# Optimization experiments

Hardware: AMD Instinct MI355X
Metric: run time of the kernel (lower is better)

Reference implementation:

```python
import jax, jax.numpy as jnp
import numpy as np

N = 50000   # nodes
E = 600000  # edges
D = 128     # embedding_size (= in_size)
OUT = 2     # out_channels
L = 12
# aggr schedule from the source: conv1..conv10, conv11, con12
AGGRS = ['sum', 'mean', 'max', 'sum', 'mean', 'max', 'sum', 'mean', 'max', 'sum', 'max', 'mean']


def setup_inputs() -> dict:
    key = jax.random.key(0)
    ks = jax.random.split(key, 8)
    s = 1.0 / np.sqrt(D)
    x = jax.random.normal(ks[0], (N, D), jnp.float32)
    edge_index = jax.random.randint(ks[1], (2, E), 0, N, jnp.int32)
    # stacked SAGEConv params: lin_l (neighbor path, with bias), lin_r (root path, no bias)
    Wl = jax.random.normal(ks[2], (L, D, D), jnp.float32) * s
    bl = jax.random.normal(ks[3], (L, D), jnp.float32) * s
    Wr = jax.random.normal(ks[4], (L, D, D), jnp.float32) * s
    W1 = jax.random.normal(ks[5], (D, D), jnp.float32) * s
    b1 = jnp.zeros((D,), jnp.float32)
    W2 = jax.random.normal(ks[6], (OUT, D), jnp.float32) * s
    b2 = jnp.zeros((OUT,), jnp.float32)
    return {"x": x, "edge_index": edge_index, "Wl": Wl, "bl": bl, "Wr": Wr,
            "W1": W1, "b1": b1, "W2": W2, "b2": b2}


def _aggregate(msgs, dst, aggr):
    # msgs: [E, D] gathered source features; scatter-reduce to [N, D]
    if aggr == 'sum':
        return jax.ops.segment_sum(msgs, dst, num_segments=N)
    if aggr == 'mean':
        s = jax.ops.segment_sum(msgs, dst, num_segments=N)
        cnt = jax.ops.segment_sum(jnp.ones((msgs.shape[0], 1), msgs.dtype), dst, num_segments=N)
        return s / jnp.maximum(cnt, 1.0)
    # max: empty segments come back -inf -> 0 (PyG convention)
    mx = jax.ops.segment_max(msgs, dst, num_segments=N)
    return jnp.where(jnp.isneginf(mx), 0.0, mx)


def reference(x, edge_index, Wl, bl, Wr, W1, b1, W2, b2):
    src, dst = edge_index[0], edge_index[1]
    h = x
    for i, aggr in enumerate(AGGRS):
        agg = _aggregate(h[src], dst, aggr)          # gather + scatter-reduce
        h = jax.nn.relu(agg @ Wl[i].T + bl[i] + h @ Wr[i].T)
        # dropout after layers 10 and 11 is identity in eval mode
    h = jax.nn.relu(h @ W1.T + b1)
    return h @ W2.T + b2
```

## Files before the change

kernel.cpp:

```cpp
#include <hip/hip_runtime.h>
#include <math.h>

#define NN 50000
#define NE 600000
#define DIM 128
#define NL 12

typedef short bf16x8 __attribute__((ext_vector_type(8)));
typedef float f32x4 __attribute__((ext_vector_type(4)));

__device__ __forceinline__ uint f2b_rne(float f) {
    uint u = __float_as_uint(f);
    return (u + 0x7fffu + ((u >> 16) & 1u)) >> 16;
}

#define NX8 (NN * DIM / 8)
#define NW8 (NL * DIM * DIM / 8)
#define NW18 (DIM * DIM / 8)
#define NCVT (NX8 + 2 * NW8 + NW18)

__global__ void prep_kernel(const float* __restrict__ x, const float* __restrict__ Wl,
                            const float* __restrict__ Wr, const float* __restrict__ W1,
                            ushort* __restrict__ xb, ushort* __restrict__ Wlb,
                            ushort* __restrict__ Wrb, ushort* __restrict__ W1b,
                            const int* __restrict__ dst, int* __restrict__ counts) {
    int i = blockIdx.x * blockDim.x + threadIdx.x;
    if (i < NE) atomicAdd(&counts[dst[i]], 1);
    const float* in; ushort* out; int off;
    if (i < NX8)                        { in = x;  out = xb;  off = i; }
    else if (i < NX8 + NW8)             { in = Wl; out = Wlb; off = i - NX8; }
    else if (i < NX8 + 2 * NW8)         { in = Wr; out = Wrb; off = i - NX8 - NW8; }
    else if (i < NCVT)                  { in = W1; out = W1b; off = i - NX8 - 2 * NW8; }
    else return;
    const float4* p = reinterpret_cast<const float4*>(in);
    float4 v0 = p[off * 2], v1 = p[off * 2 + 1];
    uint4 o;
    o.x = (f2b_rne(v0.y) << 16) | f2b_rne(v0.x);
    o.y = (f2b_rne(v0.w) << 16) | f2b_rne(v0.z);
    o.z = (f2b_rne(v1.y) << 16) | f2b_rne(v1.x);
    o.w = (f2b_rne(v1.w) << 16) | f2b_rne(v1.z);
    reinterpret_cast<uint4*>(out)[off] = o;
}

__global__ __launch_bounds__(1024) void scan1_kernel(const int* __restrict__ counts,
                                                     int* __restrict__ offsets,
                                                     int* __restrict__ bsums) {
    int b = blockIdx.x, t = threadIdx.x;
    int i = b * 1024 + t;
    int lane = t & 63, wid = t >> 6;
    int val = (i < NN) ? counts[i] : 0;
#pragma unroll
    for (int o = 1; o < 64; o <<= 1) {
        int n = __shfl_up(val, o);
        if (lane >= o) val += n;
    }
    __shared__ int ws[16];
    if (lane == 63) ws[wid] = val;
    __syncthreads();
    if (wid == 0 && lane < 16) {
        int s = ws[lane];
#pragma unroll
        for (int o = 1; o < 16; o <<= 1) {
            int n = __shfl_up(s, o);
            if (lane >= o) s += n;
        }
        ws[lane] = s;
    }
    __syncthreads();
    if (wid) val += ws[wid - 1];
    if (i < NN) offsets[i + 1] = val;
    if (t == 1023) bsums[b] = val;
}

__global__ void scan2_kernel(const int* __restrict__ bsums, int* __restrict__ bbase, int nb) {
    int lane = threadIdx.x;
    int v = (lane < nb) ? bsums[lane] : 0;
    int val = v;
#pragma unroll
    for (int o = 1; o < 64; o <<= 1) {
        int n = __shfl_up(val, o);
        if (lane >= o) val += n;
    }
    if (lane < nb) bbase[lane] = val - v;
}

__global__ void scan3_kernel(int* __restrict__ offsets, const int* __restrict__ bbase) {
    int i = blockIdx.x * blockDim.x + threadIdx.x;
    if (i == 0) { offsets[0] = 0; return; }
    if (i <= NN) offsets[i] += bbase[(i - 1) >> 10];
}

__global__ void fill_kernel(const int* __restrict__ src, const int* __restrict__ dst,
                            const int* __restrict__ offsets, int* __restrict__ cursor,
                            int* __restrict__ csr) {
    int e = blockIdx.x * blockDim.x + threadIdx.x;
    if (e < NE) {
        int d = dst[e];
        int p = atomicAdd(&cursor[d], 1);
        csr[offsets[d] + p] = src[e];
    }
}

template <int AGGR>
__global__ __launch_bounds__(256) void aggregate_kernel(
    const ushort* __restrict__ h, ushort* __restrict__ agg,
    const int* __restrict__ csr, const int* __restrict__ offsets) {
    int wid = (blockIdx.x * blockDim.x + threadIdx.x) >> 6;
    int l = threadIdx.x & 63;
    if (wid >= NN) return;
    int s0 = offsets[wid], s1 = offsets[wid + 1];
    const uint* hp = reinterpret_cast<const uint*>(h);
    float ax, ay;
    if (AGGR == 2) { ax = ay = -INFINITY; } else { ax = ay = 0.f; }
    for (int e = s0; e < s1; e += 16) {
        int rem = s1 - e;
        uint u[16];
#pragma unroll
        for (int q = 0; q < 16; ++q) {
            int ee = (q < rem) ? e + q : s1 - 1;
            uint off = (uint)csr[ee] * 64u + (uint)l;
            u[q] = hp[off];
        }
        __builtin_amdgcn_sched_barrier(0);
#pragma unroll
        for (int q = 0; q < 16; ++q) {
            if (q < rem) {
                float fx = __uint_as_float(u[q] << 16);
                float fy = __uint_as_float(u[q] & 0xffff0000u);
                if (AGGR == 2) { ax = fmaxf(ax, fx); ay = fmaxf(ay, fy); }
                else           { ax += fx;           ay += fy; }
            }
        }
    }
    int deg = s1 - s0;
    if (AGGR == 1) {
        float inv = 1.f / (float)(deg > 0 ? deg : 1);
        ax *= inv; ay *= inv;
    }
    if (AGGR == 2 && deg == 0) { ax = ay = 0.f; }
    uint o = (f2b_rne(ay) << 16) | f2b_rne(ax);
    reinterpret_cast<uint*>(agg)[(uint)wid * 64u + (uint)l] = o;
}

template <int NPASS>
__global__ __launch_bounds__(256) void gemm_kernel(
    const ushort* __restrict__ A1, const ushort* __restrict__ Wa,
    const ushort* __restrict__ A2, const ushort* __restrict__ Wb,
    const float* __restrict__ bias, ushort* __restrict__ C) {
    __shared__ ushort Wlds[NPASS][DIM * DIM];
    int t = threadIdx.x, w = t >> 6, l = t & 63;
    int lr = l & 15, lg = l >> 4;

#pragma unroll
    for (int pass = 0; pass < NPASS; ++pass) {
        const uint4* Wv = reinterpret_cast<const uint4*>(pass ? Wb : Wa);
        char* base = reinterpret_cast<char*>(Wlds[pass]);
#pragma unroll
        for (int i = 0; i < 8; ++i) {
            int chunk = t + i * 256;
            uint4 v = Wv[chunk];
            int byte = chunk << 4;
            int row = byte >> 8;
            *reinterpret_cast<uint4*>(base + (byte ^ ((row & 7) << 4))) = v;
        }
    }
    __syncthreads();

    int row0 = blockIdx.x * 128 + w * 32;
    f32x4 acc[2][8];
#pragma unroll
    for (int rf = 0; rf < 2; ++rf)
#pragma unroll
        for (int c = 0; c < 8; ++c) acc[rf][c] = (f32x4){0.f, 0.f, 0.f, 0.f};
    int grow0 = min(row0 + lr, NN - 1);
    int grow1 = min(row0 + 16 + lr, NN - 1);

#pragma unroll
    for (int pass = 0; pass < NPASS; ++pass) {
        const ushort* A = pass ? A2 : A1;
        const char* wbase = reinterpret_cast<const char*>(Wlds[pass]);
#pragma unroll
        for (int kk = 0; kk < 4; ++kk) {
            int ko = kk * 32 + lg * 8;
            bf16x8 nf0 = *reinterpret_cast<const bf16x8*>(A + (size_t)grow0 * DIM + ko);
            bf16x8 nf1 = *reinterpret_cast<const bf16x8*>(A + (size_t)grow1 * DIM + ko);
#pragma unroll
            for (int c = 0; c < 8; ++c) {
                int wbyte = (((c * 16 + lr) << 8) + (ko << 1)) ^ ((lr & 7) << 4);
                bf16x8 wf = *reinterpret_cast<const bf16x8*>(wbase + wbyte);
                acc[0][c] = __builtin_amdgcn_mfma_f32_16x16x32_bf16(wf, nf0, acc[0][c], 0, 0, 0);
                acc[1][c] = __builtin_amdgcn_mfma_f32_16x16x32_bf16(wf, nf1, acc[1][c], 0, 0, 0);
            }
        }
    }
#pragma unroll
    for (int rf = 0; rf < 2; ++rf) {
        int orow = row0 + rf * 16 + lr;
        if (orow < NN) {
#pragma unroll
            for (int c = 0; c < 8; ++c) {
                int col0 = c * 16 + lg * 4;
                float4 b4 = *reinterpret_cast<const float4*>(bias + col0);
                float v0 = fmaxf(acc[rf][c][0] + b4.x, 0.f);
                float v1 = fmaxf(acc[rf][c][1] + b4.y, 0.f);
                float v2 = fmaxf(acc[rf][c][2] + b4.z, 0.f);
                float v3 = fmaxf(acc[rf][c][3] + b4.w, 0.f);
                uint2 o;
                o.x = (f2b_rne(v1) << 16) | f2b_rne(v0);
                o.y = (f2b_rne(v3) << 16) | f2b_rne(v2);
                *reinterpret_cast<uint2*>(C + (size_t)orow * DIM + col0) = o;
            }
        }
    }
}

__global__ void out_kernel(const ushort* __restrict__ h2, const float* __restrict__ W2,
                           const float* __restrict__ b2, float* __restrict__ out) {
    int wid = (blockIdx.x * blockDim.x + threadIdx.x) >> 6;
    int lane = threadIdx.x & 63;
    if (wid >= NN) return;
    uint u = reinterpret_cast<const uint*>(h2)[(uint)wid * 64u + (uint)lane];
    float vx = __uint_as_float(u << 16), vy = __uint_as_float(u & 0xffff0000u);
    float2 w0 = *reinterpret_cast<const float2*>(W2 + lane * 2);
    float2 w1 = *reinterpret_cast<const float2*>(W2 + DIM + lane * 2);
    float s0 = vx * w0.x + vy * w0.y;
    float s1 = vx * w1.x + vy * w1.y;
    for (int off = 32; off; off >>= 1) {
        s0 += __shfl_down(s0, off);
        s1 += __shfl_down(s1, off);
    }
    if (lane == 0) {
        out[wid * 2 + 0] = s0 + b2[0];
        out[wid * 2 + 1] = s1 + b2[1];
    }
}

extern "C" void kernel_launch(void* const* d_in, const int* in_sizes, int n_in,
                              void* d_out, int out_size, void* d_ws, size_t ws_size,
                              hipStream_t stream) {
    const float* x  = (const float*)d_in[0];
    const int*   ei = (const int*)d_in[1];
    const float* Wl = (const float*)d_in[2];
    const float* bl = (const float*)d_in[3];
    const float* Wr = (const float*)d_in[4];
    const float* W1 = (const float*)d_in[5];
    const float* b1 = (const float*)d_in[6];
    const float* W2 = (const float*)d_in[7];
    const float* b2 = (const float*)d_in[8];
    float* out = (float*)d_out;

    int* counts  = (int*)d_ws;
    int* offsets = counts + NN;
    int* bsums   = offsets + NN + 1;
    int* bbase   = bsums + 64;
    int* csr     = bbase + 64;
    size_t fixed = ((size_t)(NN + NN + 1 + 128 + NE) * sizeof(int) + 255) & ~(size_t)255;
    ushort* xb   = (ushort*)((char*)d_ws + fixed);
    ushort* bufA = xb + (size_t)NN * DIM;
    ushort* bufB = bufA + (size_t)NN * DIM;
    ushort* Wlb  = bufB + (size_t)NN * DIM;
    ushort* Wrb  = Wlb + (size_t)NL * DIM * DIM;
    ushort* W1b  = Wrb + (size_t)NL * DIM * DIM;

    const int* src = ei;
    const int* dst = ei + NE;

    hipMemsetAsync(counts, 0, NN * sizeof(int), stream);
    prep_kernel<<<(NCVT + 255) / 256, 256, 0, stream>>>(x, Wl, Wr, W1, xb, Wlb, Wrb, W1b,
                                                        dst, counts);
    const int NB = (NN + 1023) / 1024;
    scan1_kernel<<<NB, 1024, 0, stream>>>(counts, offsets, bsums);
    scan2_kernel<<<1, 64, 0, stream>>>(bsums, bbase, NB);
    scan3_kernel<<<(NN + 1 + 255) / 256, 256, 0, stream>>>(offsets, bbase);
    hipMemsetAsync(counts, 0, NN * sizeof(int), stream);
    fill_kernel<<<(NE + 255) / 256, 256, 0, stream>>>(src, dst, offsets, counts, csr);

    static const int AGGRS[NL] = {0, 1, 2, 0, 1, 2, 0, 1, 2, 0, 2, 1};
    dim3 agrd((NN * 64 + 255) / 256);
    dim3 ggrd((NN + 127) / 128);
    ushort* B[3] = {xb, bufA, bufB};
    int hi = 0;
    for (int i = 0; i < NL; ++i) {
        int ai = (hi + 1) % 3, oi = (hi + 2) % 3;
        const ushort* h = B[hi];
        if (AGGRS[i] == 0)
            aggregate_kernel<0><<<agrd, 256, 0, stream>>>(h, B[ai], csr, offsets);
        else if (AGGRS[i] == 1)
            aggregate_kernel<1><<<agrd, 256, 0, stream>>>(h, B[ai], csr, offsets);
        else
            aggregate_kernel<2><<<agrd, 256, 0, stream>>>(h, B[ai], csr, offsets);
        gemm_kernel<2><<<ggrd, 256, 0, stream>>>(B[ai], Wlb + (size_t)i * DIM * DIM, h,
                                                 Wrb + (size_t)i * DIM * DIM,
                                                 bl + (size_t)i * DIM, B[oi]);
        hi = oi;
    }
    int fi = (hi + 1) % 3;
    gemm_kernel<1><<<ggrd, 256, 0, stream>>>(B[hi], W1b, nullptr, nullptr, b1, B[fi]);
    out_kernel<<<agrd, 256, 0, stream>>>(B[fi], W2, b2, out);
}
```

Baseline: 614.7 us.

## Process two nodes per wave in aggregation and reuse single LDS weight buffer in GEMM

The aggregation kernel now assigns two destination nodes to each wavefront. It loads one CSR index per lane and broadcasts it with readlane, then issues 32 independent row gathers per iteration to raise memory-level parallelism. The dual-pass GEMM now reuses a single 32KB LDS weight buffer with an extra barrier, halving LDS use so more blocks can fit per CU. The risks are wasted gathers when the two nodes differ in degree, and the added barrier between passes.

```diff
diff --git a/kernel.cpp b/kernel.cpp
--- a/kernel.cpp
+++ b/kernel.cpp
@@ -105,41 +105,66 @@
 __global__ __launch_bounds__(256) void aggregate_kernel(
     const ushort* __restrict__ h, ushort* __restrict__ agg,
     const int* __restrict__ csr, const int* __restrict__ offsets) {
-    int wid = (blockIdx.x * blockDim.x + threadIdx.x) >> 6;
+    int wv = (blockIdx.x * blockDim.x + threadIdx.x) >> 6;
     int l = threadIdx.x & 63;
-    if (wid >= NN) return;
-    int s0 = offsets[wid], s1 = offsets[wid + 1];
+    if (wv >= NN / 2) return;
+    int na = wv * 2, nb = na + 1;
+    int s0a = offsets[na], s1a = offsets[na + 1];
+    int s0b = offsets[nb], s1b = offsets[nb + 1];
     const uint* hp = reinterpret_cast<const uint*>(h);
-    float ax, ay;
-    if (AGGR == 2) { ax = ay = -INFINITY; } else { ax = ay = 0.f; }
-    for (int e = s0; e < s1; e += 16) {
-        int rem = s1 - e;
-        uint u[16];
+    float axa, aya, axb, ayb;
+    if (AGGR == 2) { axa = aya = axb = ayb = -INFINITY; } else { axa = aya = axb = ayb = 0.f; }
+    int ea = s0a, eb = s0b;
+    while (ea < s1a || eb < s1b) {
+        int rema = s1a - ea, remb = s1b - eb;
+        int q15 = l & 15;
+        int ia = max(min(ea + q15, s1a - 1), 0);
+        int ib = max(min(eb + q15, s1b - 1), 0);
+        int mycsr = csr[((l & 31) < 16) ? ia : ib];
+        uint u[32];
 #pragma unroll
         for (int q = 0; q < 16; ++q) {
-            int ee = (q < rem) ? e + q : s1 - 1;
-            uint off = (uint)csr[ee] * 64u + (uint)l;
-            u[q] = hp[off];
+            int sa = __builtin_amdgcn_readlane(mycsr, q);
+            u[q] = hp[(uint)sa * 64u + (uint)l];
+        }
+#pragma unroll
+        for (int q = 0; q < 16; ++q) {
+            int sb = __builtin_amdgcn_readlane(mycsr, 16 + q);
+            u[16 + q] = hp[(uint)sb * 64u + (uint)l];
         }
         __builtin_amdgcn_sched_barrier(0);
 #pragma unroll
         for (int q = 0; q < 16; ++q) {
-            if (q < rem) {
+            if (q < rema) {
                 float fx = __uint_as_float(u[q] << 16);
                 float fy = __uint_as_float(u[q] & 0xffff0000u);
-                if (AGGR == 2) { ax = fmaxf(ax, fx); ay = fmaxf(ay, fy); }
-                else           { ax += fx;           ay += fy; }
+                if (AGGR == 2) { axa = fmaxf(axa, fx); aya = fmaxf(aya, fy); }
+                else           { axa += fx;            aya += fy; }
             }
         }
-    }
-    int deg = s1 - s0;
+#pragma unroll
+        for (int q = 0; q < 16; ++q) {
+            if (q < remb) {
+                float fx = __uint_as_float(u[16 + q] << 16);
+                float fy = __uint_as_float(u[16 + q] & 0xffff0000u);
+                if (AGGR == 2) { axb = fmaxf(axb, fx); ayb = fmaxf(ayb, fy); }
+                else           { axb += fx;            ayb += fy; }
+            }
+        }
+        ea += 16; eb += 16;
+    }
+    int dega = s1a - s0a, degb = s1b - s0b;
     if (AGGR == 1) {
-        float inv = 1.f / (float)(deg > 0 ? deg : 1);
-        ax *= inv; ay *= inv;
-    }
-    if (AGGR == 2 && deg == 0) { ax = ay = 0.f; }
-    uint o = (f2b_rne(ay) << 16) | f2b_rne(ax);
-    reinterpret_cast<uint*>(agg)[(uint)wid * 64u + (uint)l] = o;
+        float inva = 1.f / (float)(dega > 0 ? dega : 1);
+        float invb = 1.f / (float)(degb > 0 ? degb : 1);
+        axa *= inva; aya *= inva; axb *= invb; ayb *= invb;
+    }
+    if (AGGR == 2) {
+        if (dega == 0) { axa = aya = 0.f; }
+        if (degb == 0) { axb = ayb = 0.f; }
+    }
+    reinterpret_cast<uint*>(agg)[(uint)na * 64u + (uint)l] = (f2b_rne(aya) << 16) | f2b_rne(axa);
+    reinterpret_cast<uint*>(agg)[(uint)nb * 64u + (uint)l] = (f2b_rne(ayb) << 16) | f2b_rne(axb);
 }
 
 template <int NPASS>
@@ -147,14 +172,23 @@
     const ushort* __restrict__ A1, const ushort* __restrict__ Wa,
     const ushort* __restrict__ A2, const ushort* __restrict__ Wb,
     const float* __restrict__ bias, ushort* __restrict__ C) {
-    __shared__ ushort Wlds[NPASS][DIM * DIM];
+    __shared__ ushort Wlds[DIM * DIM];
     int t = threadIdx.x, w = t >> 6, l = t & 63;
     int lr = l & 15, lg = l >> 4;
+    int row0 = blockIdx.x * 128 + w * 32;
+    f32x4 acc[2][8];
+#pragma unroll
+    for (int rf = 0; rf < 2; ++rf)
+#pragma unroll
+        for (int c = 0; c < 8; ++c) acc[rf][c] = (f32x4){0.f, 0.f, 0.f, 0.f};
+    int grow0 = min(row0 + lr, NN - 1);
+    int grow1 = min(row0 + 16 + lr, NN - 1);
 
 #pragma unroll
     for (int pass = 0; pass < NPASS; ++pass) {
+        if (pass) __syncthreads();
         const uint4* Wv = reinterpret_cast<const uint4*>(pass ? Wb : Wa);
-        char* base = reinterpret_cast<char*>(Wlds[pass]);
+        char* base = reinterpret_cast<char*>(Wlds);
 #pragma unroll
         for (int i = 0; i < 8; ++i) {
             int chunk = t + i * 256;
@@ -163,22 +197,8 @@
             int row = byte >> 8;
             *reinterpret_cast<uint4*>(base + (byte ^ ((row & 7) << 4))) = v;
         }
-    }
-    __syncthreads();
-
-    int row0 = blockIdx.x * 128 + w * 32;
-    f32x4 acc[2][8];
-#pragma unroll
-    for (int rf = 0; rf < 2; ++rf)
-#pragma unroll
-        for (int c = 0; c < 8; ++c) acc[rf][c] = (f32x4){0.f, 0.f, 0.f, 0.f};
-    int grow0 = min(row0 + lr, NN - 1);
-    int grow1 = min(row0 + 16 + lr, NN - 1);
-
-#pragma unroll
-    for (int pass = 0; pass < NPASS; ++pass) {
+        __syncthreads();
         const ushort* A = pass ? A2 : A1;
-        const char* wbase = reinterpret_cast<const char*>(Wlds[pass]);
 #pragma unroll
         for (int kk = 0; kk < 4; ++kk) {
             int ko = kk * 32 + lg * 8;
@@ -187,7 +207,7 @@
 #pragma unroll
             for (int c = 0; c < 8; ++c) {
                 int wbyte = (((c * 16 + lr) << 8) + (ko << 1)) ^ ((lr & 7) << 4);
-                bf16x8 wf = *reinterpret_cast<const bf16x8*>(wbase + wbyte);
+                bf16x8 wf = *reinterpret_cast<const bf16x8*>(base + wbyte);
                 acc[0][c] = __builtin_amdgcn_mfma_f32_16x16x32_bf16(wf, nf0, acc[0][c], 0, 0, 0);
                 acc[1][c] = __builtin_amdgcn_mfma_f32_16x16x32_bf16(wf, nf1, acc[1][c], 0, 0, 0);
             }
@@ -276,7 +296,8 @@
     fill_kernel<<<(NE + 255) / 256, 256, 0, stream>>>(src, dst, offsets, counts, csr);
 
     static const int AGGRS[NL] = {0, 1, 2, 0, 1, 2, 0, 1, 2, 0, 2, 1};
-    dim3 agrd((NN * 64 + 255) / 256);
+    dim3 agrd((NN / 2 * 64 + 255) / 256);
+    dim3 ogrd((NN * 64 + 255) / 256);
     dim3 ggrd((NN + 127) / 128);
     ushort* B[3] = {xb, bufA, bufB};
     int hi = 0;
@@ -296,5 +317,5 @@
     }
     int fi = (hi + 1) % 3;
     gemm_kernel<1><<<ggrd, 256, 0, stream>>>(B[hi], W1b, nullptr, nullptr, b1, B[fi]);
-    out_kernel<<<agrd, 256, 0, stream>>>(B[fi], W2, b2, out);
-}
+    out_kernel<<<ogrd, 256, 0, stream>>>(B[fi], W2, b2, out);
+}
```

Result: no change. 611.1 us (-0.6%).
